# Optimization experiments

Measured on AMD Instinct MI355X. Metric: run time of the kernel, lower is better.

The kernel has to match this reference:

```python
import jax, jax.numpy as jnp
import numpy as np

B, S, D, V = 4, 1024, 512, 32000
INNER, NHM, DHM, QB = 1024, 4, 256, 4   # mLSTM: proj_factor 2.0 -> inner=2*D, 4 heads
NHS, DHS, K = 4, 128, 3                  # sLSTM: 4 heads over D, causal conv k=3
EPS = 1e-5


def layernorm(x, w):
    mu = x.mean(-1, keepdims=True)
    var = ((x - mu) ** 2).mean(-1, keepdims=True)
    return (x - mu) * jax.lax.rsqrt(var + EPS) * w


def headnorm(x, w):
    # x: (B,S,NH,DH) normalize per head over DH (GroupNorm), scale by w (NH*DH,)
    mu = x.mean(-1, keepdims=True)
    var = ((x - mu) ** 2).mean(-1, keepdims=True)
    xn = (x - mu) * jax.lax.rsqrt(var + EPS)
    b, s, nh, dh = x.shape
    return xn.reshape(b, s, nh * dh) * w


def causal_conv(x, w, bias):
    # depthwise causal conv: x (B,S,C), kernel w (C,K)
    k = w.shape[1]
    s = x.shape[1]
    xp = jnp.pad(x, ((0, 0), (k - 1, 0), (0, 0)))
    y = sum(xp[:, i:i + s, :] * w[:, i] for i in range(k))
    return y + bias


def blockdiag(x, w):
    # LinearHeadwiseExpand: block-diagonal linear, w (NB, out_bs, in_bs)
    b, s, _ = x.shape
    nb, ob, ib = w.shape
    return jnp.einsum('bsni,noi->bsno', x.reshape(b, s, nb, ib), w).reshape(b, s, nb * ob)


def mlstm_parallel(q, k, v, ig, fg):
    # parallel_stabilized_simple; q,k,v (B,NH,S,DH), ig/fg (B,NH,S)
    dh = q.shape[-1]
    s = q.shape[2]
    lf = jax.nn.log_sigmoid(fg)
    cs = jnp.cumsum(lf, axis=-1)
    logfmat = cs[..., :, None] - cs[..., None, :]      # (i,j) = sum_{j+1..i} log f
    mask = jnp.tril(jnp.ones((s, s), dtype=bool))
    logD = jnp.where(mask, logfmat + ig[..., None, :], -jnp.inf)
    maxD = logD.max(-1, keepdims=True)                 # rowwise stabilizer
    Dm = jnp.exp(logD - maxD)
    C = jnp.einsum('bhid,bhjd->bhij', q, k) * (dh ** -0.5) * Dm
    norm = jnp.maximum(jnp.abs(C.sum(-1, keepdims=True)), jnp.exp(-maxD))
    return jnp.einsum('bhij,bhjd->bhid', C / (norm + 1e-6), v)


def mlstm_block(x, p):
    (ln, Wup, convW, convb, Wq, Wk, Wv, Wi, bi, Wf, bf, skip, onorm, Wdown) = p
    b, s, _ = x.shape
    xin = layernorm(x, ln) @ Wup                        # (B,S,2*INNER)
    xm, z = jnp.split(xin, 2, axis=-1)
    xc = jax.nn.silu(causal_conv(xm, convW, convb))
    q = blockdiag(xc, Wq)
    kk = blockdiag(xc, Wk)
    v = blockdiag(xm, Wv)
    qkv = jnp.concatenate([q, kk, v], axis=-1)
    ig = (qkv @ Wi + bi).transpose(0, 2, 1)             # (B,NH,S)
    fg = (qkv @ Wf + bf).transpose(0, 2, 1)
    qh = q.reshape(b, s, NHM, DHM).transpose(0, 2, 1, 3)
    kh = kk.reshape(b, s, NHM, DHM).transpose(0, 2, 1, 3)
    vh = v.reshape(b, s, NHM, DHM).transpose(0, 2, 1, 3)
    h = mlstm_parallel(qh, kh, vh, ig, fg)              # (B,NH,S,DH)
    h = headnorm(h.transpose(0, 2, 1, 3), onorm)        # (B,S,INNER)
    h = (h + skip * xc) * jax.nn.silu(z)
    return x + h @ Wdown


def slstm_block(x, p):
    (ln1, convW, convb, Wig, Wfg, Wzg, Wog, R, bias, gn, ln2, Wu, Wd) = p
    b, s, _ = x.shape
    xn = layernorm(x, ln1)
    xc = jax.nn.silu(causal_conv(xn, convW, convb))

    def gate(inp, W):  # headwise linear, W (NH, DH, DH)
        return jnp.einsum('bshi,hoi->bsho', inp.reshape(b, s, NHS, DHS), W)

    # gate preactivations, gate order i,f,z,o: (B,S,4,NH,DH)
    Wx = jnp.stack([gate(xc, Wig), gate(xc, Wfg), gate(xn, Wzg), gate(xn, Wog)], axis=2)

    def step(carry, wx):
        y, c, n, m = carry
        raw = wx + jnp.einsum('bhd,hdge->bghe', y, R) + bias
        ir, fr, zr, orr = raw[:, 0], raw[:, 1], raw[:, 2], raw[:, 3]
        lfm = m + jax.nn.log_sigmoid(fr)
        mn = jnp.maximum(ir, lfm)                        # exp-gating stabilizer
        igt = jnp.exp(ir - mn)
        fgt = jnp.exp(lfm - mn)
        cn = fgt * c + igt * jnp.tanh(zr)
        nn_ = fgt * n + igt
        yn = jax.nn.sigmoid(orr) * cn / nn_
        return (yn, cn, nn_, mn), yn

    z0 = jnp.zeros((b, NHS, DHS), x.dtype)
    _, ys = jax.lax.scan(step, (z0, z0, z0, z0), Wx.transpose(1, 0, 2, 3, 4))
    h = x + headnorm(ys.transpose(1, 0, 2, 3), gn)
    # gated feedforward (proj_factor=1.0, gelu)
    u = layernorm(h, ln2) @ Wu
    g, up = jnp.split(u, 2, axis=-1)
    return h + (jax.nn.gelu(g, approximate=False) * up) @ Wd


def forward(x, emb, m0, s1, m2, post_ln, clf_W, clf_b):
    h = emb[x]
    h = mlstm_block(h, m0)
    h = slstm_block(h, s1)
    h = mlstm_block(h, m2)
    h = layernorm(h, post_ln)
    return h[:, -1, :] @ clf_W + clf_b


def setup_inputs() -> dict:
    key = jax.random.key(0)
    ks = iter(jax.random.split(key, 64))

    def rn(shape, s=0.02):
        return jax.random.normal(next(ks), shape, jnp.float32) * s

    def mblock():
        return dict(
            ln=jnp.ones((D,)), Wup=rn((D, 2 * INNER)),
            convW=rn((INNER, K), 0.1), convb=jnp.zeros((INNER,)),
            Wq=rn((INNER // QB, QB, QB), 0.2), Wk=rn((INNER // QB, QB, QB), 0.2),
            Wv=rn((INNER // QB, QB, QB), 0.2),
            Wi=rn((3 * INNER, NHM)), bi=rn((NHM,), 0.1),
            Wf=rn((3 * INNER, NHM)), bf=jnp.linspace(3.0, 6.0, NHM),
            skip=jnp.ones((INNER,)), onorm=jnp.ones((INNER,)), Wdown=rn((INNER, D)))

    m0 = mblock()
    m2 = mblock()
    emb = rn((V, D), 1.0).at[0].set(0.0)  # padding_idx=0 row zeroed
    inp = {'x': jax.random.randint(next(ks), (B, S), 0, V), 'emb': emb}
    for pre, m in (('m0_', m0), ('m2_', m2)):
        for k_, v_ in m.items():
            inp[pre + k_] = v_
    zb = jnp.zeros((NHS, DHS))
    inp.update(
        s1_ln1=jnp.ones((D,)), s1_convW=rn((D, K), 0.1), s1_convb=jnp.zeros((D,)),
        s1_Wig=rn((NHS, DHS, DHS), 0.1), s1_Wfg=rn((NHS, DHS, DHS), 0.1),
        s1_Wzg=rn((NHS, DHS, DHS), 0.1), s1_Wog=rn((NHS, DHS, DHS), 0.1),
        s1_R=rn((NHS, DHS, 4, DHS), 0.05),
        s1_b=jnp.stack([zb, jnp.linspace(3.0, 6.0, NHS)[:, None] * jnp.ones((NHS, DHS)), zb, zb], axis=0),
        s1_gn=jnp.ones((D,)), s1_ln2=jnp.ones((D,)),
        s1_Wu=rn((D, 2 * D)), s1_Wd=rn((D, D)),
        post_ln=jnp.ones((D,)), clf_W=rn((D, 1)), clf_b=jnp.zeros((1,)))
    return inp


def reference(x, emb, m0_ln, m0_Wup, m0_convW, m0_convb, m0_Wq, m0_Wk, m0_Wv, m0_Wi, m0_bi, m0_Wf, m0_bf, m0_skip, m0_onorm, m0_Wdown,
              s1_ln1, s1_convW, s1_convb, s1_Wig, s1_Wfg, s1_Wzg, s1_Wog, s1_R, s1_b, s1_gn, s1_ln2, s1_Wu, s1_Wd,
              m2_ln, m2_Wup, m2_convW, m2_convb, m2_Wq, m2_Wk, m2_Wv, m2_Wi, m2_bi, m2_Wf, m2_bf, m2_skip, m2_onorm, m2_Wdown,
              post_ln, clf_W, clf_b):
    m0 = (m0_ln, m0_Wup, m0_convW, m0_convb, m0_Wq, m0_Wk, m0_Wv, m0_Wi, m0_bi, m0_Wf, m0_bf, m0_skip, m0_onorm, m0_Wdown)
    s1 = (s1_ln1, s1_convW, s1_convb, s1_Wig, s1_Wfg, s1_Wzg, s1_Wog, s1_R, s1_b, s1_gn, s1_ln2, s1_Wu, s1_Wd)
    m2 = (m2_ln, m2_Wup, m2_convW, m2_convb, m2_Wq, m2_Wk, m2_Wv, m2_Wi, m2_bi, m2_Wf, m2_bf, m2_skip, m2_onorm, m2_Wdown)
    return forward(x, emb, m0, s1, m2, post_ln, clf_W, clf_b)
```

## Files before the change

kernel.cpp:

```cpp
#include <hip/hip_runtime.h>
#include <cstddef>
#include <cstdint>

#define EPSV 1e-5f

typedef __attribute__((ext_vector_type(8))) short bf16x8;
typedef __attribute__((ext_vector_type(4))) float f32x4;
typedef __attribute__((ext_vector_type(2))) float f32x2;

__device__ __forceinline__ short f2bf(float f) {
  union { float f; unsigned u; } v; v.f = f;
  unsigned r = (v.u + 0x7FFFu + ((v.u >> 16) & 1u)) >> 16;
  return (short)r;
}
__device__ __forceinline__ float bf2f(short s) {
  union { unsigned u; float f; } v; v.u = ((unsigned)(unsigned short)s) << 16;
  return v.f;
}

__device__ __forceinline__ float wsum(float v) {
  v += __shfl_xor(v, 32, 64);
  v += __shfl_xor(v, 16, 64);
  v += __shfl_xor(v, 8, 64);
  v += __shfl_xor(v, 4, 64);
  v += __shfl_xor(v, 2, 64);
  v += __shfl_xor(v, 1, 64);
  return v;
}

__global__ __launch_bounds__(128) void k_embed(const int* __restrict__ x,
                                               const float* __restrict__ emb,
                                               float* __restrict__ out) {
  int t = blockIdx.x, tid = threadIdx.x;
  int row = x[t];
  const float4 v = *reinterpret_cast<const float4*>(emb + (size_t)row * 512 + tid * 4);
  *reinterpret_cast<float4*>(out + (size_t)t * 512 + tid * 4) = v;
}

__global__ __launch_bounds__(128) void k_ln512(const float* __restrict__ in,
                                               const float* __restrict__ w,
                                               float* __restrict__ outf,
                                               short* __restrict__ out16) {
  int t = blockIdx.x, tid = threadIdx.x;
  const float4 v = *reinterpret_cast<const float4*>(in + (size_t)t * 512 + tid * 4);
  float s = v.x + v.y + v.z + v.w;
  float s2 = v.x * v.x + v.y * v.y + v.z * v.z + v.w * v.w;
  s = wsum(s); s2 = wsum(s2);
  __shared__ float l1[2], l2[2];
  int wv = tid >> 6;
  if ((tid & 63) == 0) { l1[wv] = s; l2[wv] = s2; }
  __syncthreads();
  s = l1[0] + l1[1]; s2 = l2[0] + l2[1];
  float mu = s * (1.f / 512.f);
  float var = s2 * (1.f / 512.f) - mu * mu;
  float r = rsqrtf(var + EPSV);
  const float4 w4 = *reinterpret_cast<const float4*>(w + tid * 4);
  float4 o;
  o.x = (v.x - mu) * r * w4.x;
  o.y = (v.y - mu) * r * w4.y;
  o.z = (v.z - mu) * r * w4.z;
  o.w = (v.w - mu) * r * w4.w;
  if (outf) *reinterpret_cast<float4*>(outf + (size_t)t * 512 + tid * 4) = o;
  *reinterpret_cast<short4*>(out16 + (size_t)t * 512 + tid * 4) =
      make_short4(f2bf(o.x), f2bf(o.y), f2bf(o.z), f2bf(o.w));
}

template <bool OUT16, bool RES>
__global__ __launch_bounds__(256) void k_mm(
    const short* __restrict__ A, size_t sA1, size_t sA2, int lda,
    const short* __restrict__ B, size_t sB1, size_t sB2, int ldb,
    const float* __restrict__ Res, size_t sR1, size_t sR2, int ldr,
    void* __restrict__ Cv, size_t sC1, size_t sC2, int ldc,
    int K, int HB) {
  const int z = blockIdx.z, zh = z / HB, zl = z - zh * HB;
  A += zh * sA1 + zl * sA2;
  B += zh * sB1 + zl * sB2;
  const int bm = blockIdx.y * 128, bn = blockIdx.x * 128;
  const int tid = threadIdx.x, lane = tid & 63, w = tid >> 6;
  const int wr = w >> 1, wc = w & 1;
  const int l15 = lane & 15, l4 = lane >> 4;
  __shared__ short As[128 * 72];
  __shared__ short Bs[128 * 72];
  f32x4 acc[4][4];
#pragma unroll
  for (int i = 0; i < 4; ++i)
#pragma unroll
    for (int j = 0; j < 4; ++j) acc[i][j] = (f32x4){0.f, 0.f, 0.f, 0.f};
  const int srow = tid >> 3, sg = tid & 7;
  for (int k0 = 0; k0 < K; k0 += 64) {
    int4 ra[4], rb[4];
#pragma unroll
    for (int it = 0; it < 4; ++it) {
      int row = it * 32 + srow;
      ra[it] = *reinterpret_cast<const int4*>(A + (size_t)(bm + row) * lda + k0 + sg * 8);
      rb[it] = *reinterpret_cast<const int4*>(B + (size_t)(bn + row) * ldb + k0 + sg * 8);
    }
    __syncthreads();
#pragma unroll
    for (int it = 0; it < 4; ++it) {
      int row = it * 32 + srow;
      *reinterpret_cast<int4*>(As + row * 72 + sg * 8) = ra[it];
      *reinterpret_cast<int4*>(Bs + row * 72 + sg * 8) = rb[it];
    }
    __syncthreads();
#pragma unroll
    for (int kk = 0; kk < 2; ++kk) {
      bf16x8 af[4], bfr[4];
#pragma unroll
      for (int i = 0; i < 4; ++i) {
        af[i]  = *reinterpret_cast<const bf16x8*>(As + (wr * 64 + i * 16 + l15) * 72 + kk * 32 + l4 * 8);
        bfr[i] = *reinterpret_cast<const bf16x8*>(Bs + (wc * 64 + i * 16 + l15) * 72 + kk * 32 + l4 * 8);
      }
#pragma unroll
      for (int i = 0; i < 4; ++i)
#pragma unroll
        for (int j = 0; j < 4; ++j)
          acc[i][j] = __builtin_amdgcn_mfma_f32_16x16x32_bf16(af[i], bfr[j], acc[i][j], 0, 0, 0);
    }
  }
  const int row0 = bm + wr * 64 + l4 * 4, col0 = bn + wc * 64 + l15;
  if constexpr (OUT16) {
    short* C = (short*)Cv + zh * sC1 + zl * sC2;
#pragma unroll
    for (int mi = 0; mi < 4; ++mi)
#pragma unroll
      for (int r = 0; r < 4; ++r) {
        size_t ro = (size_t)(row0 + mi * 16 + r) * ldc;
#pragma unroll
        for (int ni = 0; ni < 4; ++ni) C[ro + col0 + ni * 16] = f2bf(acc[mi][ni][r]);
      }
  } else {
    float* C = (float*)Cv + zh * sC1 + zl * sC2;
    const float* Rp = Res ? (Res + zh * sR1 + zl * sR2) : nullptr;
#pragma unroll
    for (int mi = 0; mi < 4; ++mi)
#pragma unroll
      for (int r = 0; r < 4; ++r) {
        int rw = row0 + mi * 16 + r;
#pragma unroll
        for (int ni = 0; ni < 4; ++ni) {
          float vv = acc[mi][ni][r];
          if constexpr (RES) vv += Rp[(size_t)rw * ldr + col0 + ni * 16];
          C[(size_t)rw * ldc + col0 + ni * 16] = vv;
        }
      }
  }
}

__global__ __launch_bounds__(256) void k_transp(const float* __restrict__ in, size_t sI1, size_t sI2, int ldi,
                                                short* __restrict__ out, size_t sO1, size_t sO2, int ldo,
                                                int HB) {
  __shared__ float t[32][33];
  int z = blockIdx.z, zh = z / HB, zl = z - zh * HB;
  in += zh * sI1 + zl * sI2;
  out += zh * sO1 + zl * sO2;
  int r0 = blockIdx.x * 32, c0 = blockIdx.y * 32;
  int tx = threadIdx.x & 31, ty = threadIdx.x >> 5;
#pragma unroll
  for (int i = 0; i < 4; ++i) {
    int rr = ty + i * 8;
    t[rr][tx] = in[(size_t)(r0 + rr) * ldi + c0 + tx];
  }
  __syncthreads();
#pragma unroll
  for (int i = 0; i < 4; ++i) {
    int cr = ty + i * 8;
    out[(size_t)(c0 + cr) * ldo + r0 + tx] = f2bf(t[tx][cr]);
  }
}

__global__ __launch_bounds__(256) void k_conv_silu(const float* __restrict__ in, int inLd, int logC,
                                                   const float* __restrict__ w,
                                                   const float* __restrict__ bias,
                                                   float* __restrict__ out,
                                                   short* __restrict__ out16) {
  int idx = blockIdx.x * 256 + threadIdx.x;
  int C = 1 << logC;
  int t = idx >> logC, c = idx & (C - 1);
  int s = t & 1023;
  const float* ip = in + (size_t)t * inLd + c;
  float acc = bias[c] + w[c * 3 + 2] * ip[0];
  if (s >= 1) acc += w[c * 3 + 1] * ip[-(ptrdiff_t)inLd];
  if (s >= 2) acc += w[c * 3 + 0] * ip[-2 * (ptrdiff_t)inLd];
  float r = acc / (1.f + __expf(-acc));
  out[(size_t)t * C + c] = r;
  if (out16) out16[(size_t)t * C + c] = f2bf(r);
}

__global__ __launch_bounds__(256) void k_qkv(const float* __restrict__ xc, const float* __restrict__ x2,
                                             const float* __restrict__ Wq, const float* __restrict__ Wk,
                                             const float* __restrict__ Wv,
                                             float* __restrict__ q, float* __restrict__ k,
                                             float* __restrict__ v,
                                             short* __restrict__ q16, short* __restrict__ k16) {
  int t = blockIdx.x, n = threadIdx.x;
  const float4 xcv = *reinterpret_cast<const float4*>(xc + (size_t)t * 1024 + n * 4);
  const float4 xmv = *reinterpret_cast<const float4*>(x2 + (size_t)t * 2048 + n * 4);
  float qa[4], ka[4], va[4];
#pragma unroll
  for (int o = 0; o < 4; ++o) {
    const float4 wq = *reinterpret_cast<const float4*>(Wq + n * 16 + o * 4);
    const float4 wk = *reinterpret_cast<const float4*>(Wk + n * 16 + o * 4);
    const float4 wv = *reinterpret_cast<const float4*>(Wv + n * 16 + o * 4);
    qa[o] = xcv.x * wq.x + xcv.y * wq.y + xcv.z * wq.z + xcv.w * wq.w;
    ka[o] = xcv.x * wk.x + xcv.y * wk.y + xcv.z * wk.z + xcv.w * wk.w;
    va[o] = xmv.x * wv.x + xmv.y * wv.y + xmv.z * wv.z + xmv.w * wv.w;
  }
  *reinterpret_cast<float4*>(q + (size_t)t * 1024 + n * 4) = make_float4(qa[0], qa[1], qa[2], qa[3]);
  *reinterpret_cast<float4*>(k + (size_t)t * 1024 + n * 4) = make_float4(ka[0], ka[1], ka[2], ka[3]);
  *reinterpret_cast<float4*>(v + (size_t)t * 1024 + n * 4) = make_float4(va[0], va[1], va[2], va[3]);
  *reinterpret_cast<short4*>(q16 + (size_t)t * 1024 + n * 4) =
      make_short4(f2bf(qa[0]), f2bf(qa[1]), f2bf(qa[2]), f2bf(qa[3]));
  *reinterpret_cast<short4*>(k16 + (size_t)t * 1024 + n * 4) =
      make_short4(f2bf(ka[0]), f2bf(ka[1]), f2bf(ka[2]), f2bf(ka[3]));
}

__global__ __launch_bounds__(256) void k_igfg(const float* __restrict__ q, const float* __restrict__ k,
                                              const float* __restrict__ v,
                                              const float* __restrict__ Wi, const float* __restrict__ bi,
                                              const float* __restrict__ Wf, const float* __restrict__ bf,
                                              float* __restrict__ ig, float* __restrict__ fg) {
  int t = blockIdx.x, tid = threadIdx.x;
  float aI[4] = {0.f, 0.f, 0.f, 0.f}, aF[4] = {0.f, 0.f, 0.f, 0.f};
  for (int c = tid; c < 1024; c += 256) {
    float qv = q[(size_t)t * 1024 + c];
    float kv = k[(size_t)t * 1024 + c];
    float vv = v[(size_t)t * 1024 + c];
    const float4 wiq = *reinterpret_cast<const float4*>(Wi + (size_t)c * 4);
    const float4 wik = *reinterpret_cast<const float4*>(Wi + (size_t)(1024 + c) * 4);
    const float4 wiv = *reinterpret_cast<const float4*>(Wi + (size_t)(2048 + c) * 4);
    const float4 wfq = *reinterpret_cast<const float4*>(Wf + (size_t)c * 4);
    const float4 wfk = *reinterpret_cast<const float4*>(Wf + (size_t)(1024 + c) * 4);
    const float4 wfv = *reinterpret_cast<const float4*>(Wf + (size_t)(2048 + c) * 4);
    aI[0] += qv * wiq.x + kv * wik.x + vv * wiv.x;
    aI[1] += qv * wiq.y + kv * wik.y + vv * wiv.y;
    aI[2] += qv * wiq.z + kv * wik.z + vv * wiv.z;
    aI[3] += qv * wiq.w + kv * wik.w + vv * wiv.w;
    aF[0] += qv * wfq.x + kv * wfk.x + vv * wfv.x;
    aF[1] += qv * wfq.y + kv * wfk.y + vv * wfv.y;
    aF[2] += qv * wfq.z + kv * wfk.z + vv * wfv.z;
    aF[3] += qv * wfq.w + kv * wfk.w + vv * wfv.w;
  }
#pragma unroll
  for (int h = 0; h < 4; ++h) { aI[h] = wsum(aI[h]); aF[h] = wsum(aF[h]); }
  __shared__ float red[2][4][4];
  int wv = tid >> 6;
  if ((tid & 63) == 0) {
#pragma unroll
    for (int h = 0; h < 4; ++h) { red[0][wv][h] = aI[h]; red[1][wv][h] = aF[h]; }
  }
  __syncthreads();
  if (tid < 8) {
    int which = tid >> 2, h = tid & 3;
    float sum = red[which][0][h] + red[which][1][h] + red[which][2][h] + red[which][3][h];
    int b = t >> 10, s = t & 1023;
    size_t o = (size_t)(b * 4 + h) * 1024 + s;
    if (which == 0) ig[o] = sum + bi[h];
    else            fg[o] = sum + bf[h];
  }
}

__global__ __launch_bounds__(1024) void k_gatescan(const float* __restrict__ ig, const float* __restrict__ fg,
                                                   float* __restrict__ a, float* __restrict__ Mx,
                                                   float* __restrict__ emax) {
  int bh = blockIdx.x, s = threadIdx.x;
  size_t o = (size_t)bh * 1024 + s;
  float f = fg[o];
  float lf = (f >= 0.f) ? -log1pf(__expf(-f)) : (f - log1pf(__expf(f)));
  __shared__ float buf[1024];
  float val = lf;
  buf[s] = val;
  __syncthreads();
#pragma unroll
  for (int off = 1; off < 1024; off <<= 1) {
    float add = (s >= off) ? buf[s - off] : 0.f;
    __syncthreads();
    val += add; buf[s] = val;
    __syncthreads();
  }
  float csv = val;
  float av = ig[o] - csv;
  float mv = av;
  buf[s] = mv;
  __syncthreads();
#pragma unroll
  for (int off = 1; off < 1024; off <<= 1) {
    float other = (s >= off) ? buf[s - off] : -3.4e38f;
    __syncthreads();
    mv = fmaxf(mv, other); buf[s] = mv;
    __syncthreads();
  }
  a[o] = av;
  Mx[o] = mv;
  emax[o] = __expf(-(csv + mv));
}

__global__ __launch_bounds__(256) void k_mask(short* __restrict__ P, const float* __restrict__ a,
                                              const float* __restrict__ Mx, const float* __restrict__ emax,
                                              int bhBase) {
  int i = blockIdx.x, z = blockIdx.y, tid = threadIdx.x;
  int bh = bhBase + z;
  short* Prow = P + ((size_t)z * 1024 + i) * 1024;
  const float* ab = a + (size_t)bh * 1024;
  float Mi = Mx[(size_t)bh * 1024 + i];
  float vals[4];
  float rs = 0.f;
#pragma unroll
  for (int jj = 0; jj < 4; ++jj) {
    int j = tid + jj * 256;
    float pv = 0.f;
    if (j <= i) pv = bf2f(Prow[j]) * 0.0625f * __expf(ab[j] - Mi);
    vals[jj] = pv;
    rs += pv;
  }
  rs = wsum(rs);
  __shared__ float red[4];
  if ((tid & 63) == 0) red[tid >> 6] = rs;
  __syncthreads();
  float tot = red[0] + red[1] + red[2] + red[3];
  float norm = fmaxf(fabsf(tot), emax[(size_t)bh * 1024 + i]) + 1e-6f;
  float inv = 1.f / norm;
#pragma unroll
  for (int jj = 0; jj < 4; ++jj) Prow[tid + jj * 256] = f2bf(vals[jj] * inv);
}

__global__ __launch_bounds__(256) void k_hncomb(const float* __restrict__ hattn, const float* __restrict__ xc,
                                                const float* __restrict__ x2, const float* __restrict__ onorm,
                                                const float* __restrict__ skip, short* __restrict__ out) {
  int t = blockIdx.x, tid = threadIdx.x;
  int w = tid >> 6, lane = tid & 63;
  int cbase = w * 256 + lane * 4;
  const float4 v = *reinterpret_cast<const float4*>(hattn + (size_t)t * 1024 + cbase);
  float s = v.x + v.y + v.z + v.w;
  float s2 = v.x * v.x + v.y * v.y + v.z * v.z + v.w * v.w;
  s = wsum(s); s2 = wsum(s2);
  float mu = s * (1.f / 256.f), var = s2 * (1.f / 256.f) - mu * mu;
  float r = rsqrtf(var + EPSV);
  const float4 on4 = *reinterpret_cast<const float4*>(onorm + cbase);
  const float4 sk4 = *reinterpret_cast<const float4*>(skip + cbase);
  const float4 xc4 = *reinterpret_cast<const float4*>(xc + (size_t)t * 1024 + cbase);
  const float4 z4 = *reinterpret_cast<const float4*>(x2 + (size_t)t * 2048 + 1024 + cbase);
  float4 o;
  o.x = ((v.x - mu) * r * on4.x + sk4.x * xc4.x) * (z4.x / (1.f + __expf(-z4.x)));
  o.y = ((v.y - mu) * r * on4.y + sk4.y * xc4.y) * (z4.y / (1.f + __expf(-z4.y)));
  o.z = ((v.z - mu) * r * on4.z + sk4.z * xc4.z) * (z4.z / (1.f + __expf(-z4.z)));
  o.w = ((v.w - mu) * r * on4.w + sk4.w * xc4.w) * (z4.w / (1.f + __expf(-z4.w)));
  *reinterpret_cast<short4*>(out + (size_t)t * 1024 + cbase) =
      make_short4(f2bf(o.x), f2bf(o.y), f2bf(o.z), f2bf(o.w));
}

__global__ __launch_bounds__(256) void k_wcat(const float* __restrict__ wi, const float* __restrict__ wf,
                                              const float* __restrict__ wz, const float* __restrict__ wo,
                                              short* __restrict__ Wcat) {
  int idx = blockIdx.x * 256 + threadIdx.x;
  int g = idx >> 16, r = idx & 65535;
  const float* s = (g == 0) ? wi : ((g == 1) ? wf : ((g == 2) ? wz : wo));
  Wcat[idx] = f2bf(s[r]);
}

__global__ __launch_bounds__(512, 1) void k_scan(const float* __restrict__ Wx, const float* __restrict__ R,
                                                 const float* __restrict__ bias, float* __restrict__ ys) {
  int bh = blockIdx.x, b = bh >> 2, h = bh & 3;
  int tid = threadIdx.x;
  int e = tid >> 2, g = tid & 3;
  f32x2 rc[64];
  {
    const float* Rp = R + (size_t)h * 65536 + g * 128 + e;
#pragma unroll
    for (int i = 0; i < 64; ++i) {
      rc[i][0] = Rp[(size_t)(2 * i) * 512];
      rc[i][1] = Rp[(size_t)(2 * i + 1) * 512];
    }
  }
  const float bsv = bias[(size_t)g * 512 + h * 128 + e];
  const float* wxp = Wx + (size_t)b * 1024 * 2048 + h * 512 + g * 128 + e;
  __shared__ float ysh[2][128];
  if (tid < 128) { ysh[0][tid] = 0.f; ysh[1][tid] = 0.f; }
  float c_ = 0.f, n_ = 0.f, m_ = 0.f;
  float wx = wxp[0];
  float* ysg = ys + ((size_t)b * 1024) * 512 + h * 128 + e;
  __syncthreads();
  for (int s = 0; s < 1024; ++s) {
    const float* yb = &ysh[(s + 1) & 1][0];
    int sp = (s + 1 < 1024) ? (s + 1) : 1023;
    float wxn = wxp[(size_t)sp * 2048];
    f32x2 accA = {0.f, 0.f}, accB = {0.f, 0.f};
#pragma unroll
    for (int i = 0; i < 32; ++i) {
      const f32x2 y0 = *reinterpret_cast<const f32x2*>(yb + i * 4);
      const f32x2 y1 = *reinterpret_cast<const f32x2*>(yb + i * 4 + 2);
      accA = y0 * rc[2 * i] + accA;
      accB = y1 * rc[2 * i + 1] + accB;
    }
    float raw = ((accA[0] + accB[0]) + (accA[1] + accB[1])) + wx + bsv;
    float o1 = __shfl_xor(raw, 1, 64);
    float o2 = __shfl_xor(raw, 2, 64);
    float o3 = __shfl_xor(o1, 2, 64);
    const bool g0 = (g & 1) != 0, g1 = (g & 2) != 0;
    float ir  = g1 ? (g0 ? o3 : o2) : (g0 ? o1 : raw);
    float fr  = g1 ? (g0 ? o2 : o3) : (g0 ? raw : o1);
    float zr  = g1 ? (g0 ? o1 : raw) : (g0 ? o3 : o2);
    float orr = g1 ? (g0 ? raw : o1) : (g0 ? o2 : o3);
    float lsf = (fr >= 0.f) ? -__logf(1.f + __expf(-fr)) : (fr - __logf(1.f + __expf(fr)));
    float lfm = m_ + lsf;
    float mn = fmaxf(ir, lfm);
    float igt = __expf(ir - mn);
    float fgt = __expf(lfm - mn);
    float t2 = __expf(-2.f * fabsf(zr));
    float th = (1.f - t2) / (1.f + t2);
    th = (zr >= 0.f) ? th : -th;
    float cn = fgt * c_ + igt * th;
    float nn = fgt * n_ + igt;
    float yn = cn / (nn * (1.f + __expf(-orr)));
    c_ = cn; n_ = nn; m_ = mn;
    if (g == 0) {
      ysh[s & 1][e] = yn;
      ysg[(size_t)s * 512] = yn;
    }
    wx = wxn;
    __syncthreads();
  }
}

__global__ __launch_bounds__(512) void k_hnadd(const float* __restrict__ hin, const float* __restrict__ ysv,
                                               const float* __restrict__ gn, float* __restrict__ out) {
  int t = blockIdx.x, tid = threadIdx.x;
  float yv = ysv[(size_t)t * 512 + tid];
  float s = wsum(yv), s2 = wsum(yv * yv);
  __shared__ float l1[8], l2[8];
  int wv = tid >> 6;
  if ((tid & 63) == 0) { l1[wv] = s; l2[wv] = s2; }
  __syncthreads();
  int h2 = (tid >> 7) * 2;
  float S = l1[h2] + l1[h2 + 1], S2 = l2[h2] + l2[h2 + 1];
  float mu = S * (1.f / 128.f), var = S2 * (1.f / 128.f) - mu * mu;
  float r = rsqrtf(var + EPSV);
  out[(size_t)t * 512 + tid] = hin[(size_t)t * 512 + tid] + (yv - mu) * r * gn[tid];
}

__global__ __launch_bounds__(256) void k_geluprod(const float* __restrict__ u, short* __restrict__ gp) {
  int idx = blockIdx.x * 256 + threadIdx.x;
  int t = idx >> 9, c = idx & 511;
  float g = u[(size_t)t * 1024 + c];
  float up = u[(size_t)t * 1024 + 512 + c];
  float ge = 0.5f * g * (1.f + erff(g * 0.70710678118654752f));
  gp[idx] = f2bf(ge * up);
}

__global__ __launch_bounds__(128) void k_final(const float* __restrict__ h, const float* __restrict__ w,
                                               const float* __restrict__ cw, const float* __restrict__ cb,
                                               float* __restrict__ out) {
  int b = blockIdx.x, tid = threadIdx.x;
  const float* row = h + ((size_t)(b * 1024 + 1023)) * 512;
  const float4 v = *reinterpret_cast<const float4*>(row + tid * 4);
  float s = v.x + v.y + v.z + v.w;
  float s2 = v.x * v.x + v.y * v.y + v.z * v.z + v.w * v.w;
  s = wsum(s); s2 = wsum(s2);
  __shared__ float l1[2], l2[2];
  int wv = tid >> 6;
  if ((tid & 63) == 0) { l1[wv] = s; l2[wv] = s2; }
  __syncthreads();
  s = l1[0] + l1[1]; s2 = l2[0] + l2[1];
  float mu = s * (1.f / 512.f);
  float var = s2 * (1.f / 512.f) - mu * mu;
  float r = rsqrtf(var + EPSV);
  const float4 w4 = *reinterpret_cast<const float4*>(w + tid * 4);
  const float4 c4 = *reinterpret_cast<const float4*>(cw + tid * 4);
  float d = (v.x - mu) * r * w4.x * c4.x + (v.y - mu) * r * w4.y * c4.y +
            (v.z - mu) * r * w4.z * c4.z + (v.w - mu) * r * w4.w * c4.w;
  d = wsum(d);
  __syncthreads();
  if ((tid & 63) == 0) l1[tid >> 6] = d;
  __syncthreads();
  if (tid == 0) out[b] = l1[0] + l1[1] + cb[0];
}

extern "C" void kernel_launch(void* const* d_in, const int* in_sizes, int n_in,
                              void* d_out, int out_size, void* d_ws, size_t ws_size,
                              hipStream_t stream) {
  (void)in_sizes; (void)n_in; (void)out_size; (void)ws_size;
  auto F = [&](int i) { return (const float*)d_in[i]; };
  const int* x = (const int*)d_in[0];
  const float* emb = F(1);

  float* ws = (float*)d_ws;
  size_t off = 0;
  auto alloc = [&](size_t n) { float* p = ws + off; off += n; return p; };
  float* hA = alloc(2097152);
  float* hB = alloc(2097152);
  float* X2 = alloc(8388608);
  float* C1 = alloc(4194304);
  float* C2 = alloc(4194304);
  float* C3 = alloc(4194304);
  float* C4 = alloc(4194304);
  float* C5 = alloc(4194304);
  float* g_a = alloc(16384);
  float* g_M = alloc(16384);
  float* g_e = alloc(16384);
  float* g_ig = alloc(16384);
  float* g_fg = alloc(16384);
  short* q16 = (short*)alloc(2097152);
  short* k16 = (short*)alloc(2097152);
  short* A16a = (short*)alloc(1048576);
  short* A16b = (short*)alloc(1048576);
  short* WT = (short*)alloc(524288);
  short* Wc16 = (short*)alloc(131072);
  short* Pb16 = (short*)C2;
  short* VT = (short*)C3;
  short* H16 = (short*)q16;

  k_embed<<<4096, 128, 0, stream>>>(x, emb, hA);

  auto mlstm = [&](int pi, const float* hin, float* hout) {
    const float* ln = F(pi);       const float* Wup = F(pi + 1);
    const float* convW = F(pi + 2); const float* convb = F(pi + 3);
    const float* Wq = F(pi + 4);   const float* Wk = F(pi + 5);  const float* Wv = F(pi + 6);
    const float* Wi = F(pi + 7);   const float* bi = F(pi + 8);
    const float* Wf = F(pi + 9);   const float* bf_ = F(pi + 10);
    const float* skip = F(pi + 11); const float* onorm = F(pi + 12);
    const float* Wdown = F(pi + 13);

    k_ln512<<<4096, 128, 0, stream>>>(hin, ln, nullptr, A16a);
    k_transp<<<dim3(16, 64, 1), 256, 0, stream>>>(Wup, 0, 0, 2048, WT, 0, 0, 512, 1);
    k_mm<false, false><<<dim3(16, 32, 1), 256, 0, stream>>>(
        A16a, 0, 0, 512, WT, 0, 0, 512, nullptr, 0, 0, 0, X2, 0, 0, 2048, 512, 1);
    k_conv_silu<<<(4096 * 1024) / 256, 256, 0, stream>>>(X2, 2048, 10, convW, convb, C1, nullptr);
    k_qkv<<<4096, 256, 0, stream>>>(C1, X2, Wq, Wk, Wv, C2, C3, C4, q16, k16);
    k_igfg<<<4096, 256, 0, stream>>>(C2, C3, C4, Wi, bi, Wf, bf_, g_ig, g_fg);
    k_gatescan<<<16, 1024, 0, stream>>>(g_ig, g_fg, g_a, g_M, g_e);
    k_transp<<<dim3(32, 8, 16), 256, 0, stream>>>(C4, 1048576, 256, 1024, VT, 1048576, 262144, 1024, 4);
    for (int c = 0; c < 2; ++c) {
      const short* qc = q16 + (size_t)c * 2097152;
      const short* kc = k16 + (size_t)c * 2097152;
      k_mm<true, false><<<dim3(8, 8, 8), 256, 0, stream>>>(
          qc, 1048576, 256, 1024, kc, 1048576, 256, 1024,
          nullptr, 0, 0, 0, Pb16, 4194304, 1048576, 1024, 256, 4);
      k_mask<<<dim3(1024, 8), 256, 0, stream>>>(Pb16, g_a, g_M, g_e, c * 8);
      k_mm<false, false><<<dim3(2, 8, 8), 256, 0, stream>>>(
          Pb16, 4194304, 1048576, 1024, VT + (size_t)c * 8 * 262144, 1048576, 262144, 1024,
          nullptr, 0, 0, 0, C5 + (size_t)c * 2097152, 1048576, 256, 1024, 1024, 4);
    }
    k_hncomb<<<4096, 256, 0, stream>>>(C5, C1, X2, onorm, skip, H16);
    k_transp<<<dim3(32, 16, 1), 256, 0, stream>>>(Wdown, 0, 0, 512, WT, 0, 0, 1024, 1);
    k_mm<false, true><<<dim3(4, 32, 1), 256, 0, stream>>>(
        H16, 0, 0, 1024, WT, 0, 0, 1024, hin, 0, 0, 512, hout, 0, 0, 512, 1024, 1);
  };

  auto slstm = [&](const float* hin, float* hout) {
    const float* ln1 = F(30); const float* convW = F(31); const float* convb = F(32);
    const float* Wig = F(33); const float* Wfg = F(34); const float* Wzg = F(35);
    const float* Wog = F(36); const float* Rr = F(37);  const float* bias = F(38);
    const float* gn = F(39);  const float* ln2 = F(40);
    const float* Wu = F(41);  const float* Wd = F(42);

    k_ln512<<<4096, 128, 0, stream>>>(hin, ln1, C3, A16a);
    k_conv_silu<<<(4096 * 512) / 256, 256, 0, stream>>>(C3, 512, 9, convW, convb, C4, A16b);
    k_wcat<<<(4 * 65536) / 256, 256, 0, stream>>>(Wig, Wfg, Wzg, Wog, Wc16);
    k_mm<false, false><<<dim3(1, 32, 8), 256, 0, stream>>>(
        A16b, 128, 0, 512, Wc16, 16384, 65536, 128,
        nullptr, 0, 0, 0, X2, 512, 128, 2048, 128, 2);
    k_mm<false, false><<<dim3(1, 32, 8), 256, 0, stream>>>(
        A16a, 128, 0, 512, Wc16 + 131072, 16384, 65536, 128,
        nullptr, 0, 0, 0, X2 + 256, 512, 128, 2048, 128, 2);
    k_scan<<<16, 512, 0, stream>>>(X2, Rr, bias, C2);
    k_hnadd<<<4096, 512, 0, stream>>>(hin, C2, gn, C3);
    k_ln512<<<4096, 128, 0, stream>>>(C3, ln2, nullptr, A16a);
    k_transp<<<dim3(16, 32, 1), 256, 0, stream>>>(Wu, 0, 0, 1024, WT, 0, 0, 512, 1);
    k_mm<false, false><<<dim3(8, 32, 1), 256, 0, stream>>>(
        A16a, 0, 0, 512, WT, 0, 0, 512, nullptr, 0, 0, 0, C5, 0, 0, 1024, 512, 1);
    k_geluprod<<<(4096 * 512) / 256, 256, 0, stream>>>(C5, A16b);
    k_transp<<<dim3(16, 16, 1), 256, 0, stream>>>(Wd, 0, 0, 512, WT, 0, 0, 512, 1);
    k_mm<false, true><<<dim3(4, 32, 1), 256, 0, stream>>>(
        A16b, 0, 0, 512, WT, 0, 0, 512, C3, 0, 0, 512, hout, 0, 0, 512, 512, 1);
  };

  mlstm(2, hA, hB);
  slstm(hB, hA);
  mlstm(16, hA, hB);
  k_final<<<4, 128, 0, stream>>>(hB, F(43), F(44), F(45), (float*)d_out);
}
```

Measured before the change: 1.943 ms.

## Fuse gate projections into qkv kernel and restructure sLSTM scan reduction

Merges the igfg gate-projection kernel into the qkv kernel so the q/k/v values in registers feed the input/forget gate reductions directly. This drops the fp32 q and k global writes and the re-reads of q, k and v. Separately, the sLSTM scan now gives each lane a quarter of the recurrent dot product for all four gates instead of one full gate. It reads 128-bit chunks of the shared-memory state and combines partials with xor-shuffle adds, where before lanes exchanged finished gate values. Register pressure and shuffle count per step change, which could hurt the serial scan loop.

```diff
diff --git a/kernel.cpp b/kernel.cpp
--- a/kernel.cpp
+++ b/kernel.cpp
@@ -187,12 +187,14 @@
   if (out16) out16[(size_t)t * C + c] = f2bf(r);
 }
 
-__global__ __launch_bounds__(256) void k_qkv(const float* __restrict__ xc, const float* __restrict__ x2,
-                                             const float* __restrict__ Wq, const float* __restrict__ Wk,
-                                             const float* __restrict__ Wv,
-                                             float* __restrict__ q, float* __restrict__ k,
-                                             float* __restrict__ v,
-                                             short* __restrict__ q16, short* __restrict__ k16) {
+__global__ __launch_bounds__(256) void k_qkvig(const float* __restrict__ xc, const float* __restrict__ x2,
+                                               const float* __restrict__ Wq, const float* __restrict__ Wk,
+                                               const float* __restrict__ Wv,
+                                               const float* __restrict__ Wi, const float* __restrict__ bi,
+                                               const float* __restrict__ Wf, const float* __restrict__ bf,
+                                               float* __restrict__ v,
+                                               short* __restrict__ q16, short* __restrict__ k16,
+                                               float* __restrict__ ig, float* __restrict__ fg) {
   int t = blockIdx.x, n = threadIdx.x;
   const float4 xcv = *reinterpret_cast<const float4*>(xc + (size_t)t * 1024 + n * 4);
   const float4 xmv = *reinterpret_cast<const float4*>(x2 + (size_t)t * 2048 + n * 4);
@@ -206,52 +208,41 @@
     ka[o] = xcv.x * wk.x + xcv.y * wk.y + xcv.z * wk.z + xcv.w * wk.w;
     va[o] = xmv.x * wv.x + xmv.y * wv.y + xmv.z * wv.z + xmv.w * wv.w;
   }
-  *reinterpret_cast<float4*>(q + (size_t)t * 1024 + n * 4) = make_float4(qa[0], qa[1], qa[2], qa[3]);
-  *reinterpret_cast<float4*>(k + (size_t)t * 1024 + n * 4) = make_float4(ka[0], ka[1], ka[2], ka[3]);
   *reinterpret_cast<float4*>(v + (size_t)t * 1024 + n * 4) = make_float4(va[0], va[1], va[2], va[3]);
   *reinterpret_cast<short4*>(q16 + (size_t)t * 1024 + n * 4) =
       make_short4(f2bf(qa[0]), f2bf(qa[1]), f2bf(qa[2]), f2bf(qa[3]));
   *reinterpret_cast<short4*>(k16 + (size_t)t * 1024 + n * 4) =
       make_short4(f2bf(ka[0]), f2bf(ka[1]), f2bf(ka[2]), f2bf(ka[3]));
-}
-
-__global__ __launch_bounds__(256) void k_igfg(const float* __restrict__ q, const float* __restrict__ k,
-                                              const float* __restrict__ v,
-                                              const float* __restrict__ Wi, const float* __restrict__ bi,
-                                              const float* __restrict__ Wf, const float* __restrict__ bf,
-                                              float* __restrict__ ig, float* __restrict__ fg) {
-  int t = blockIdx.x, tid = threadIdx.x;
   float aI[4] = {0.f, 0.f, 0.f, 0.f}, aF[4] = {0.f, 0.f, 0.f, 0.f};
-  for (int c = tid; c < 1024; c += 256) {
-    float qv = q[(size_t)t * 1024 + c];
-    float kv = k[(size_t)t * 1024 + c];
-    float vv = v[(size_t)t * 1024 + c];
+#pragma unroll
+  for (int j = 0; j < 4; ++j) {
+    int c = n * 4 + j;
     const float4 wiq = *reinterpret_cast<const float4*>(Wi + (size_t)c * 4);
     const float4 wik = *reinterpret_cast<const float4*>(Wi + (size_t)(1024 + c) * 4);
     const float4 wiv = *reinterpret_cast<const float4*>(Wi + (size_t)(2048 + c) * 4);
     const float4 wfq = *reinterpret_cast<const float4*>(Wf + (size_t)c * 4);
     const float4 wfk = *reinterpret_cast<const float4*>(Wf + (size_t)(1024 + c) * 4);
     const float4 wfv = *reinterpret_cast<const float4*>(Wf + (size_t)(2048 + c) * 4);
-    aI[0] += qv * wiq.x + kv * wik.x + vv * wiv.x;
-    aI[1] += qv * wiq.y + kv * wik.y + vv * wiv.y;
-    aI[2] += qv * wiq.z + kv * wik.z + vv * wiv.z;
-    aI[3] += qv * wiq.w + kv * wik.w + vv * wiv.w;
-    aF[0] += qv * wfq.x + kv * wfk.x + vv * wfv.x;
-    aF[1] += qv * wfq.y + kv * wfk.y + vv * wfv.y;
-    aF[2] += qv * wfq.z + kv * wfk.z + vv * wfv.z;
-    aF[3] += qv * wfq.w + kv * wfk.w + vv * wfv.w;
+    aI[0] += qa[j] * wiq.x + ka[j] * wik.x + va[j] * wiv.x;
+    aI[1] += qa[j] * wiq.y + ka[j] * wik.y + va[j] * wiv.y;
+    aI[2] += qa[j] * wiq.z + ka[j] * wik.z + va[j] * wiv.z;
+    aI[3] += qa[j] * wiq.w + ka[j] * wik.w + va[j] * wiv.w;
+    aF[0] += qa[j] * wfq.x + ka[j] * wfk.x + va[j] * wfv.x;
+    aF[1] += qa[j] * wfq.y + ka[j] * wfk.y + va[j] * wfv.y;
+    aF[2] += qa[j] * wfq.z + ka[j] * wfk.z + va[j] * wfv.z;
+    aF[3] += qa[j] * wfq.w + ka[j] * wfk.w + va[j] * wfv.w;
   }
 #pragma unroll
   for (int h = 0; h < 4; ++h) { aI[h] = wsum(aI[h]); aF[h] = wsum(aF[h]); }
   __shared__ float red[2][4][4];
-  int wv = tid >> 6;
-  if ((tid & 63) == 0) {
-#pragma unroll
-    for (int h = 0; h < 4; ++h) { red[0][wv][h] = aI[h]; red[1][wv][h] = aF[h]; }
-  }
-  __syncthreads();
-  if (tid < 8) {
-    int which = tid >> 2, h = tid & 3;
+  int wv2 = n >> 6;
+  if ((n & 63) == 0) {
+#pragma unroll
+    for (int h = 0; h < 4; ++h) { red[0][wv2][h] = aI[h]; red[1][wv2][h] = aF[h]; }
+  }
+  __syncthreads();
+  if (n < 8) {
+    int which = n >> 2, h = n & 3;
     float sum = red[which][0][h] + red[which][1][h] + red[which][2][h] + red[which][3][h];
     int b = t >> 10, s = t & 1023;
     size_t o = (size_t)(b * 4 + h) * 1024 + s;
@@ -362,18 +353,26 @@
                                                  const float* __restrict__ bias, float* __restrict__ ys) {
   int bh = blockIdx.x, b = bh >> 2, h = bh & 3;
   int tid = threadIdx.x;
-  int e = tid >> 2, g = tid & 3;
-  f32x2 rc[64];
+  int e = tid >> 2, q = tid & 3;
+  f32x2 rc0[16], rc1[16], rc2[16], rc3[16];
   {
-    const float* Rp = R + (size_t)h * 65536 + g * 128 + e;
-#pragma unroll
-    for (int i = 0; i < 64; ++i) {
-      rc[i][0] = Rp[(size_t)(2 * i) * 512];
-      rc[i][1] = Rp[(size_t)(2 * i + 1) * 512];
-    }
-  }
-  const float bsv = bias[(size_t)g * 512 + h * 128 + e];
-  const float* wxp = Wx + (size_t)b * 1024 * 2048 + h * 512 + g * 128 + e;
+    const float* Rp = R + (size_t)h * 65536 + (size_t)(q * 32) * 512 + e;
+#pragma unroll
+    for (int i = 0; i < 16; ++i) {
+      const float* p0 = Rp + (size_t)(2 * i) * 512;
+      const float* p1 = Rp + (size_t)(2 * i + 1) * 512;
+      rc0[i][0] = p0[0];   rc0[i][1] = p1[0];
+      rc1[i][0] = p0[128]; rc1[i][1] = p1[128];
+      rc2[i][0] = p0[256]; rc2[i][1] = p1[256];
+      rc3[i][0] = p0[384]; rc3[i][1] = p1[384];
+    }
+  }
+#pragma unroll
+  for (int i = 0; i < 16; ++i)
+    asm volatile("" : "+v"(rc0[i]), "+v"(rc1[i]), "+v"(rc2[i]), "+v"(rc3[i]));
+
+  const float addb = bias[(size_t)q * 512 + h * 128 + e];
+  const float* wxp = Wx + (size_t)b * 1024 * 2048 + h * 512 + q * 128 + e;
   __shared__ float ysh[2][128];
   if (tid < 128) { ysh[0][tid] = 0.f; ysh[1][tid] = 0.f; }
   float c_ = 0.f, n_ = 0.f, m_ = 0.f;
@@ -381,26 +380,34 @@
   float* ysg = ys + ((size_t)b * 1024) * 512 + h * 128 + e;
   __syncthreads();
   for (int s = 0; s < 1024; ++s) {
-    const float* yb = &ysh[(s + 1) & 1][0];
+    const float* yq = &ysh[(s + 1) & 1][q * 32];
     int sp = (s + 1 < 1024) ? (s + 1) : 1023;
     float wxn = wxp[(size_t)sp * 2048];
-    f32x2 accA = {0.f, 0.f}, accB = {0.f, 0.f};
-#pragma unroll
-    for (int i = 0; i < 32; ++i) {
-      const f32x2 y0 = *reinterpret_cast<const f32x2*>(yb + i * 4);
-      const f32x2 y1 = *reinterpret_cast<const f32x2*>(yb + i * 4 + 2);
-      accA = y0 * rc[2 * i] + accA;
-      accB = y1 * rc[2 * i + 1] + accB;
-    }
-    float raw = ((accA[0] + accB[0]) + (accA[1] + accB[1])) + wx + bsv;
-    float o1 = __shfl_xor(raw, 1, 64);
-    float o2 = __shfl_xor(raw, 2, 64);
-    float o3 = __shfl_xor(o1, 2, 64);
-    const bool g0 = (g & 1) != 0, g1 = (g & 2) != 0;
-    float ir  = g1 ? (g0 ? o3 : o2) : (g0 ? o1 : raw);
-    float fr  = g1 ? (g0 ? o2 : o3) : (g0 ? raw : o1);
-    float zr  = g1 ? (g0 ? o1 : raw) : (g0 ? o3 : o2);
-    float orr = g1 ? (g0 ? raw : o1) : (g0 ? o2 : o3);
+    f32x2 p0 = {0.f, 0.f}, p1 = {0.f, 0.f}, p2 = {0.f, 0.f}, p3 = {0.f, 0.f};
+#pragma unroll
+    for (int i = 0; i < 8; ++i) {
+      const f32x4 y4 = *reinterpret_cast<const f32x4*>(yq + i * 4);
+      const f32x2 yA = {y4[0], y4[1]};
+      const f32x2 yB = {y4[2], y4[3]};
+      p0 = yA * rc0[2 * i] + p0;  p0 = yB * rc0[2 * i + 1] + p0;
+      p1 = yA * rc1[2 * i] + p1;  p1 = yB * rc1[2 * i + 1] + p1;
+      p2 = yA * rc2[2 * i] + p2;  p2 = yB * rc2[2 * i + 1] + p2;
+      p3 = yA * rc3[2 * i] + p3;  p3 = yB * rc3[2 * i + 1] + p3;
+    }
+    float pr0 = p0[0] + p0[1];
+    float pr1 = p1[0] + p1[1];
+    float pr2 = p2[0] + p2[1];
+    float pr3 = p3[0] + p3[1];
+    float add = wx + addb;
+    pr0 += (q == 0) ? add : 0.f;
+    pr1 += (q == 1) ? add : 0.f;
+    pr2 += (q == 2) ? add : 0.f;
+    pr3 += (q == 3) ? add : 0.f;
+    pr0 += __shfl_xor(pr0, 1, 64); pr1 += __shfl_xor(pr1, 1, 64);
+    pr2 += __shfl_xor(pr2, 1, 64); pr3 += __shfl_xor(pr3, 1, 64);
+    pr0 += __shfl_xor(pr0, 2, 64); pr1 += __shfl_xor(pr1, 2, 64);
+    pr2 += __shfl_xor(pr2, 2, 64); pr3 += __shfl_xor(pr3, 2, 64);
+    float ir = pr0, fr = pr1, zr = pr2, orr = pr3;
     float lsf = (fr >= 0.f) ? -__logf(1.f + __expf(-fr)) : (fr - __logf(1.f + __expf(fr)));
     float lfm = m_ + lsf;
     float mn = fmaxf(ir, lfm);
@@ -413,7 +420,7 @@
     float nn = fgt * n_ + igt;
     float yn = cn / (nn * (1.f + __expf(-orr)));
     c_ = cn; n_ = nn; m_ = mn;
-    if (g == 0) {
+    if (q == 0) {
       ysh[s & 1][e] = yn;
       ysg[(size_t)s * 512] = yn;
     }
@@ -525,8 +532,7 @@
     k_mm<false, false><<<dim3(16, 32, 1), 256, 0, stream>>>(
         A16a, 0, 0, 512, WT, 0, 0, 512, nullptr, 0, 0, 0, X2, 0, 0, 2048, 512, 1);
     k_conv_silu<<<(4096 * 1024) / 256, 256, 0, stream>>>(X2, 2048, 10, convW, convb, C1, nullptr);
-    k_qkv<<<4096, 256, 0, stream>>>(C1, X2, Wq, Wk, Wv, C2, C3, C4, q16, k16);
-    k_igfg<<<4096, 256, 0, stream>>>(C2, C3, C4, Wi, bi, Wf, bf_, g_ig, g_fg);
+    k_qkvig<<<4096, 256, 0, stream>>>(C1, X2, Wq, Wk, Wv, Wi, bi, Wf, bf_, C4, q16, k16, g_ig, g_fg);
     k_gatescan<<<16, 1024, 0, stream>>>(g_ig, g_fg, g_a, g_M, g_e);
     k_transp<<<dim3(32, 8, 16), 256, 0, stream>>>(C4, 1048576, 256, 1024, VT, 1048576, 262144, 1024, 4);
     for (int c = 0; c < 2; ++c) {
```

New measurement: 1.892 ms. 2.6% less time.
